# Optimization experiments

Hardware: AMD Instinct MI355X
Metric: run time of the kernel (lower is better)

## Reference

```python
import jax, jax.numpy as jnp
import numpy as np

B, L, D, H = 4, 1024, 256, 8
TEMP = float(np.sqrt(D))
EPS_SM = 1e-6
EPS_LN = 1e-5


def setup_inputs() -> dict:
    key = jax.random.key(0)
    ks = jax.random.split(key, 8)
    std = float(np.sqrt(2.0 / (D * 2)))
    return {
        "q": jax.random.normal(ks[0], (B, L, D), jnp.float32),
        "mask": jax.random.randint(ks[1], (B, L, L), 0, 2, jnp.int32),
        "k": jax.random.normal(ks[2], (B, L, D), jnp.float32),
        "v": jax.random.normal(ks[3], (B, L, D), jnp.float32),
        "w_qs": jax.random.normal(ks[4], (H * D, D), jnp.float32) * std,
        "w_ks": jax.random.normal(ks[5], (H * D, D), jnp.float32) * std,
        "w_vs": jax.random.normal(ks[6], (H * D, D), jnp.float32) * std,
        "fc_w": jax.random.normal(ks[7], (D, H * D), jnp.float32) * float(np.sqrt(2.0 / (D + H * D))),
        "fc_b": jnp.zeros((D,), jnp.float32),
        "ln_g": jnp.ones((D,), jnp.float32),
        "ln_b": jnp.zeros((D,), jnp.float32),
    }


def masked_softmax(x, m):
    # repo's layers.masked_softmax: clamp, mask-mul, stable exp, mask-mul, normalize
    x = jnp.clip(x, -15.0, 15.0) * m
    e = jnp.exp(x - jnp.max(x, axis=-1, keepdims=True)) * m
    return e / (jnp.sum(e, axis=-1, keepdims=True) + EPS_SM)


def reference(q, mask, k, v, w_qs, w_ks, w_vs, fc_w, fc_b, ln_g, ln_b):
    residual = q
    m = mask.astype(q.dtype)[:, None, :, :]          # [B,1,Lq,Lk]
    # projections to per-head full-dim: [B,L,H,D]
    qh = (q @ w_qs.T).reshape(B, L, H, D)
    kh = (k @ w_ks.T).reshape(B, L, H, D)
    vh = (v @ w_vs.T).reshape(B, L, H, D)
    scores = jnp.einsum("bqhd,bkhd->bhqk", qh, kh) / TEMP   # [B,H,Lq,Lk]
    attn = masked_softmax(scores, m)
    out = jnp.einsum("bhqk,bkhd->bqhd", attn, vh).reshape(B, L, H * D)
    out = out @ fc_w.T + fc_b                         # [B,L,D]
    out = out + residual
    mu = jnp.mean(out, axis=-1, keepdims=True)
    var = jnp.var(out, axis=-1, keepdims=True)
    out = (out - mu) / jnp.sqrt(var + EPS_LN) * ln_g + ln_b
    # match torch attn layout: [H*B, Lq, Lk] (head-major)
    attn_hb = jnp.transpose(attn, (1, 0, 2, 3)).reshape(H * B, L, L)
    return out, attn_hb
```

## Files before the change

kernel.cpp:

```cpp
#include <hip/hip_runtime.h>
#include <cstdint>
#include <math.h>

#define Bsz 4
#define Lsz 1024
#define Dsz 256
#define Hsz 8
#define HD  2048
#define NROWS (Bsz*Lsz)
#define INV_TEMP 0.0625f

typedef __attribute__((ext_vector_type(8))) short bf16x8;
typedef __attribute__((ext_vector_type(4))) float f32x4;

__device__ inline unsigned short f2bf(float f) {
    union { float f; unsigned u; } x; x.f = f;
    unsigned r = x.u + 0x7fffu + ((x.u >> 16) & 1u);
    return (unsigned short)(r >> 16);
}
__device__ inline float bf2f(unsigned short u) {
    union { unsigned u; float f; } x; x.u = (unsigned)u << 16; return x.f;
}

#define GBL(p) ((const __attribute__((address_space(1))) unsigned int*)(p))
#define LDS(p) ((__attribute__((address_space(3))) unsigned int*)(p))

template <int TMv, int TNv, typename OutT, int EPI, int MINW>
__global__ __launch_bounds__(256, MINW) void gemm_bt(
    const unsigned short* __restrict__ A, const unsigned short* __restrict__ Bm,
    OutT* __restrict__ C,
    int K, int lda, int ldb, int ldc, int inner,
    long long sA1, long long sA2, long long sB1, long long sB2,
    long long sC1, long long sC2, float alpha,
    const int* __restrict__ mask, long long sM2,
    const float* __restrict__ invs, long long sI1, long long sI2)
{
    constexpr int WMv = TMv / 2, WNv = TNv / 2;
    constexpr int IT = TMv / 32, JT = TNv / 32;
    constexpr int APASS = TMv / 32, NPASS = (TMv + TNv) / 32;

    const int z  = blockIdx.z;
    const int i1 = z / inner;
    const int i2 = z % inner;
    A  += (size_t)i1 * sA1 + (size_t)i2 * sA2;
    Bm += (size_t)i1 * sB1 + (size_t)i2 * sB2;
    C  += (size_t)i1 * sC1 + (size_t)i2 * sC2;
    if (EPI == 1) mask += (size_t)i2 * sM2;
    if (EPI == 2) invs += (size_t)i1 * sI1 + (size_t)i2 * sI2;

    __shared__ unsigned short S[(TMv + TNv) * 64];
    unsigned short* As = S;
    unsigned short* Bs = S + TMv * 64;

    const int t    = threadIdx.x;
    const int lane = t & 63;
    const int w    = t >> 6;
    const int wm   = w & 1;
    const int wn   = w >> 1;
    const int m0   = blockIdx.x * TMv;
    const int n0   = blockIdx.y * TNv;

    const int rA = t >> 3;
    const int ch = (((t & 7) ^ (rA & 7))) * 8;
    const unsigned short* gA = A  + (size_t)(m0 + rA) * lda + ch;
    const unsigned short* gB = Bm + (size_t)(n0 + rA) * ldb + ch;

    const int fr = lane & 15;
    const int q  = lane >> 4;

    f32x4 acc[IT][JT];
#pragma unroll
    for (int i = 0; i < IT; ++i)
#pragma unroll
        for (int j = 0; j < JT; ++j) acc[i][j] = (f32x4){0.f, 0.f, 0.f, 0.f};

    for (int k0 = 0; k0 < K; k0 += 64) {
#pragma unroll
        for (int p = 0; p < NPASS; ++p) {
            const unsigned short* src = (p < APASS)
                ? (gA + (size_t)p * 32 * lda + k0)
                : (gB + (size_t)(p - APASS) * 32 * ldb + k0);
            __builtin_amdgcn_global_load_lds(GBL(src), LDS(S + p * 2048 + t * 8), 16, 0, 0);
        }
        __syncthreads();

#pragma unroll
        for (int ks = 0; ks < 2; ++ks) {
            const int slot = ((ks * 4 + q) ^ (fr & 7)) * 8;
            bf16x8 a[IT], b[JT];
#pragma unroll
            for (int i = 0; i < IT; ++i)
                a[i] = *(const bf16x8*)(As + (wm * WMv + i * 16 + fr) * 64 + slot);
#pragma unroll
            for (int j = 0; j < JT; ++j)
                b[j] = *(const bf16x8*)(Bs + (wn * WNv + j * 16 + fr) * 64 + slot);
#pragma unroll
            for (int i = 0; i < IT; ++i)
#pragma unroll
                for (int j = 0; j < JT; ++j)
                    acc[i][j] = __builtin_amdgcn_mfma_f32_16x16x32_bf16(a[i], b[j], acc[i][j], 0, 0, 0);
        }
        __syncthreads();
    }

#pragma unroll
    for (int i = 0; i < IT; ++i) {
#pragma unroll
        for (int r = 0; r < 4; ++r) {
            const int row = m0 + wm * WMv + i * 16 + q * 4 + r;
#pragma unroll
            for (int j = 0; j < JT; ++j) {
                const int col = n0 + wn * WNv + j * 16 + fr;
                float vv = acc[i][j][r] * alpha;
                if (EPI == 0) {
                    if constexpr (sizeof(OutT) == 4)
                        C[(size_t)row * ldc + col] = (OutT)vv;
                    else
                        ((unsigned short*)C)[(size_t)row * ldc + col] = f2bf(vv);
                } else if (EPI == 1) {
                    const float m = (float)mask[(size_t)row * Lsz + col];
                    vv = fminf(fmaxf(vv, -15.f), 15.f) * m;
                    vv = __expf(vv) * m;
                    ((unsigned short*)C)[(size_t)row * ldc + col] = f2bf(vv);
                } else {
                    vv *= invs[row];
                    ((unsigned short*)C)[(size_t)row * ldc + col] = f2bf(vv);
                }
            }
        }
    }
}

__global__ __launch_bounds__(256) void cast_all(
    const float* __restrict__ q, const float* __restrict__ k, const float* __restrict__ v,
    const float* __restrict__ wq, const float* __restrict__ wk, const float* __restrict__ wv,
    const float* __restrict__ fw,
    unsigned short* __restrict__ qb, unsigned short* __restrict__ kb, unsigned short* __restrict__ vb,
    unsigned short* __restrict__ wqb, unsigned short* __restrict__ wkb, unsigned short* __restrict__ wvb,
    unsigned short* __restrict__ fwb)
{
    const int gid = blockIdx.x * 256 + threadIdx.x;
    const int NQ = 262144;
    const int NW = 131072;
    const float* src; unsigned short* dst; int off;
    if      (gid < NQ)            { src = q;  dst = qb;  off = gid; }
    else if (gid < 2 * NQ)        { src = k;  dst = kb;  off = gid - NQ; }
    else if (gid < 3 * NQ)        { src = v;  dst = vb;  off = gid - 2 * NQ; }
    else if (gid < 3 * NQ + NW)   { src = wq; dst = wqb; off = gid - 3 * NQ; }
    else if (gid < 3 * NQ + 2*NW) { src = wk; dst = wkb; off = gid - 3 * NQ - NW; }
    else if (gid < 3 * NQ + 3*NW) { src = wv; dst = wvb; off = gid - 3 * NQ - 2 * NW; }
    else                          { src = fw; dst = fwb; off = gid - 3 * NQ - 3 * NW; }
    float4 f = ((const float4*)src)[off];
    ushort4 o;
    o.x = f2bf(f.x); o.y = f2bf(f.y); o.z = f2bf(f.z); o.w = f2bf(f.w);
    ((ushort4*)dst)[off] = o;
}

__global__ __launch_bounds__(256) void norm_kernel(const unsigned short* __restrict__ e,
                                                   float* __restrict__ attn,
                                                   float* __restrict__ invsum)
{
    const int r    = blockIdx.x * 4 + (threadIdx.x >> 6);
    const int lane = threadIdx.x & 63;
    const unsigned short* rowp = e + (size_t)r * Lsz + lane * 16;

    union { uint4 v[2]; unsigned short u[16]; } buf;
    buf.v[0] = *(const uint4*)rowp;
    buf.v[1] = *(const uint4*)(rowp + 8);

    float f[16];
    float s = 0.f;
#pragma unroll
    for (int i = 0; i < 16; ++i) { f[i] = bf2f(buf.u[i]); s += f[i]; }
#pragma unroll
    for (int o = 1; o <= 32; o <<= 1) s += __shfl_xor(s, o, 64);
    const float inv = 1.0f / (s + 1e-6f);

    float* op = attn + (size_t)r * Lsz + lane * 16;
#pragma unroll
    for (int c = 0; c < 4; ++c) {
        float4 o4;
        o4.x = f[c * 4 + 0] * inv; o4.y = f[c * 4 + 1] * inv;
        o4.z = f[c * 4 + 2] * inv; o4.w = f[c * 4 + 3] * inv;
        *(float4*)(op + c * 4) = o4;
    }
    if (lane == 0) invsum[r] = inv;
}

__global__ __launch_bounds__(256) void ln_kernel(const float* __restrict__ gout,
                                                 const float* __restrict__ qin,
                                                 const float* __restrict__ fc_b,
                                                 const float* __restrict__ ln_g,
                                                 const float* __restrict__ ln_b,
                                                 float* __restrict__ out)
{
    const int row = blockIdx.x;
    const int t = threadIdx.x;
    const size_t idx = (size_t)row * Dsz + t;
    const size_t P = (size_t)NROWS * Dsz;
    const float val = gout[idx] + gout[idx + P] + gout[idx + 2 * P] + gout[idx + 3 * P]
                    + fc_b[t] + qin[idx];

    __shared__ float red[4];
    float s = val;
#pragma unroll
    for (int o = 32; o > 0; o >>= 1) s += __shfl_down(s, o, 64);
    const int lane = t & 63, w = t >> 6;
    if (lane == 0) red[w] = s;
    __syncthreads();
    const float mu = (red[0] + red[1] + red[2] + red[3]) * (1.0f / Dsz);
    __syncthreads();

    float d = val - mu;
    float s2 = d * d;
#pragma unroll
    for (int o = 32; o > 0; o >>= 1) s2 += __shfl_down(s2, o, 64);
    if (lane == 0) red[w] = s2;
    __syncthreads();
    const float var = (red[0] + red[1] + red[2] + red[3]) * (1.0f / Dsz);

    out[idx] = d * rsqrtf(var + 1e-5f) * ln_g[t] + ln_b[t];
}

extern "C" void kernel_launch(void* const* d_in, const int* in_sizes, int n_in,
                              void* d_out, int out_size, void* d_ws, size_t ws_size,
                              hipStream_t stream)
{
    const float* q    = (const float*)d_in[0];
    const int*   mask = (const int*)d_in[1];
    const float* k    = (const float*)d_in[2];
    const float* v    = (const float*)d_in[3];
    const float* w_qs = (const float*)d_in[4];
    const float* w_ks = (const float*)d_in[5];
    const float* w_vs = (const float*)d_in[6];
    const float* fc_w = (const float*)d_in[7];
    const float* fc_b = (const float*)d_in[8];
    const float* ln_g = (const float*)d_in[9];
    const float* ln_b = (const float*)d_in[10];

    float* out  = (float*)d_out;
    float* attn = (float*)d_out + (size_t)NROWS * Dsz;

    unsigned short* wsu = (unsigned short*)d_ws;
    unsigned short* qh     = wsu;
    unsigned short* kh     = qh + (size_t)NROWS * HD;
    unsigned short* q_bf   = kh + (size_t)NROWS * HD;
    unsigned short* k_bf   = q_bf + (size_t)NROWS * Dsz;
    unsigned short* v_bf   = k_bf + (size_t)NROWS * Dsz;
    unsigned short* wq_bf  = v_bf + (size_t)NROWS * Dsz;
    unsigned short* wk_bf  = wq_bf + (size_t)HD * Dsz;
    unsigned short* wv_bf  = wk_bf + (size_t)HD * Dsz;
    unsigned short* vt     = wv_bf + (size_t)HD * Dsz;
    unsigned short* attn_e = vt + (size_t)Bsz * HD * Lsz;
    unsigned short* attnv  = attn_e + (size_t)32 * Lsz * Lsz;
    unsigned short* fcw_bf = attnv + (size_t)NROWS * HD;
    float*          invsum = (float*)(fcw_bf + (size_t)Dsz * HD);
    float*          fcout  = invsum + 32768;

    dim3 blk(256);

    cast_all<<<dim3(5120), blk, 0, stream>>>(q, k, v, w_qs, w_ks, w_vs, fc_w,
                                             q_bf, k_bf, v_bf, wq_bf, wk_bf, wv_bf, fcw_bf);

    {
        dim3 grid(NROWS / 64, HD / 256, 2);
        gemm_bt<64, 256, unsigned short, 0, 3><<<grid, blk, 0, stream>>>(q_bf, wq_bf, qh,
            Dsz, Dsz, Dsz, HD, 2,
            0, (long long)NROWS * Dsz, 0, (long long)HD * Dsz, 0, (long long)NROWS * HD,
            1.0f, nullptr, 0, nullptr, 0, 0);
    }

    {
        dim3 grid(HD / 64, Lsz / 256, Bsz);
        gemm_bt<64, 256, unsigned short, 0, 3><<<grid, blk, 0, stream>>>(wv_bf, v_bf, vt,
            Dsz, Dsz, Dsz, Lsz, 1,
            0, 0, (long long)Lsz * Dsz, 0, (long long)HD * Lsz, 0,
            1.0f, nullptr, 0, nullptr, 0, 0);
    }

    {
        dim3 grid(Lsz / 128, Lsz / 256, Hsz * Bsz);
        gemm_bt<128, 256, unsigned short, 1, 2><<<grid, blk, 0, stream>>>(qh, kh, attn_e,
            Dsz, HD, HD, Lsz, Bsz,
            Dsz, (long long)Lsz * HD, Dsz, (long long)Lsz * HD,
            (long long)Bsz * Lsz * Lsz, (long long)Lsz * Lsz,
            INV_TEMP, mask, (long long)Lsz * Lsz, nullptr, 0, 0);
    }

    norm_kernel<<<dim3(32 * Lsz / 4), blk, 0, stream>>>(attn_e, attn, invsum);

    {
        dim3 grid(Lsz / 64, Dsz / 256, Hsz * Bsz);
        gemm_bt<64, 256, unsigned short, 2, 3><<<grid, blk, 0, stream>>>(attn_e, vt, attnv,
            Lsz, Lsz, Lsz, HD, Bsz,
            (long long)Bsz * Lsz * Lsz, (long long)Lsz * Lsz,
            (long long)Dsz * Lsz, (long long)HD * Lsz,
            Dsz, (long long)Lsz * HD,
            1.0f, nullptr, 0, invsum, (long long)Bsz * Lsz, (long long)Lsz);
    }

    {
        dim3 grid(NROWS / 64, Dsz / 256, 4);
        gemm_bt<64, 256, float, 0, 3><<<grid, blk, 0, stream>>>(attnv, fcw_bf, fcout,
            512, HD, HD, Dsz, 4,
            0, 512, 0, 512, 0, (long long)NROWS * Dsz,
            1.0f, nullptr, 0, nullptr, 0, 0);
    }

    ln_kernel<<<dim3(NROWS), blk, 0, stream>>>(fcout, q, fc_b, ln_g, ln_b, out);
}
```

Measured before the change: 349.4 us.

## Add double-buffered LDS pipelining, bf16 mask precast, and retune GEMM tiles

Adds an optional double-buffered main loop to the shared GEMM kernel, so the global-to-LDS load of the next K tile is issued while the current tile is multiplied, removing one barrier per iteration. The int32 mask is converted to a bf16 0/1 array inside the cast kernel, which halves the mask bytes the score GEMM epilogue reads. Tile shapes for all GEMMs change to 128x128 (64x128 for the fc projection) with adjusted occupancy hints. The double-buffered variant doubles LDS per block, which may lower occupancy, and the cast kernel now also reads the full 4M-element mask.

```diff
diff --git a/kernel.cpp b/kernel.cpp
--- a/kernel.cpp
+++ b/kernel.cpp
@@ -25,19 +25,20 @@
 #define GBL(p) ((const __attribute__((address_space(1))) unsigned int*)(p))
 #define LDS(p) ((__attribute__((address_space(3))) unsigned int*)(p))
 
-template <int TMv, int TNv, typename OutT, int EPI, int MINW>
+template <int TMv, int TNv, typename OutT, int EPI, int MINW, int DB>
 __global__ __launch_bounds__(256, MINW) void gemm_bt(
     const unsigned short* __restrict__ A, const unsigned short* __restrict__ Bm,
     OutT* __restrict__ C,
     int K, int lda, int ldb, int ldc, int inner,
     long long sA1, long long sA2, long long sB1, long long sB2,
     long long sC1, long long sC2, float alpha,
-    const int* __restrict__ mask, long long sM2,
+    const unsigned short* __restrict__ maskb, long long sM2,
     const float* __restrict__ invs, long long sI1, long long sI2)
 {
     constexpr int WMv = TMv / 2, WNv = TNv / 2;
     constexpr int IT = TMv / 32, JT = TNv / 32;
     constexpr int APASS = TMv / 32, NPASS = (TMv + TNv) / 32;
+    constexpr int TILE = (TMv + TNv) * 64;
 
     const int z  = blockIdx.z;
     const int i1 = z / inner;
@@ -45,12 +46,10 @@
     A  += (size_t)i1 * sA1 + (size_t)i2 * sA2;
     Bm += (size_t)i1 * sB1 + (size_t)i2 * sB2;
     C  += (size_t)i1 * sC1 + (size_t)i2 * sC2;
-    if (EPI == 1) mask += (size_t)i2 * sM2;
-    if (EPI == 2) invs += (size_t)i1 * sI1 + (size_t)i2 * sI2;
-
-    __shared__ unsigned short S[(TMv + TNv) * 64];
-    unsigned short* As = S;
-    unsigned short* Bs = S + TMv * 64;
+    if (EPI == 1) maskb += (size_t)i2 * sM2;
+    if (EPI == 2) invs  += (size_t)i1 * sI1 + (size_t)i2 * sI2;
+
+    __shared__ unsigned short S[(DB ? 2 : 1) * TILE];
 
     const int t    = threadIdx.x;
     const int lane = t & 63;
@@ -61,7 +60,7 @@
     const int n0   = blockIdx.y * TNv;
 
     const int rA = t >> 3;
-    const int ch = (((t & 7) ^ (rA & 7))) * 8;
+    const int ch = ((t & 7) ^ (rA & 7)) * 8;
     const unsigned short* gA = A  + (size_t)(m0 + rA) * lda + ch;
     const unsigned short* gB = Bm + (size_t)(n0 + rA) * ldb + ch;
 
@@ -74,16 +73,17 @@
 #pragma unroll
         for (int j = 0; j < JT; ++j) acc[i][j] = (f32x4){0.f, 0.f, 0.f, 0.f};
 
-    for (int k0 = 0; k0 < K; k0 += 64) {
+    auto stage = [&](unsigned short* Sb, int k0) {
 #pragma unroll
         for (int p = 0; p < NPASS; ++p) {
             const unsigned short* src = (p < APASS)
                 ? (gA + (size_t)p * 32 * lda + k0)
                 : (gB + (size_t)(p - APASS) * 32 * ldb + k0);
-            __builtin_amdgcn_global_load_lds(GBL(src), LDS(S + p * 2048 + t * 8), 16, 0, 0);
-        }
-        __syncthreads();
-
+            __builtin_amdgcn_global_load_lds(GBL(src), LDS(Sb + p * 2048 + t * 8), 16, 0, 0);
+        }
+    };
+    auto kstep = [&](const unsigned short* As) {
+        const unsigned short* Bs = As + TMv * 64;
 #pragma unroll
         for (int ks = 0; ks < 2; ++ks) {
             const int slot = ((ks * 4 + q) ^ (fr & 7)) * 8;
@@ -100,7 +100,26 @@
                 for (int j = 0; j < JT; ++j)
                     acc[i][j] = __builtin_amdgcn_mfma_f32_16x16x32_bf16(a[i], b[j], acc[i][j], 0, 0, 0);
         }
+    };
+
+    if constexpr (DB) {
+        const int nk = K >> 6;
+        stage(S, 0);
         __syncthreads();
+        int cur = 0;
+        for (int kt = 0; kt < nk; ++kt) {
+            if (kt + 1 < nk) stage(S + (cur ^ 1) * TILE, (kt + 1) << 6);
+            kstep(S + cur * TILE);
+            __syncthreads();
+            cur ^= 1;
+        }
+    } else {
+        for (int k0 = 0; k0 < K; k0 += 64) {
+            stage(S, k0);
+            __syncthreads();
+            kstep(S);
+            __syncthreads();
+        }
     }
 
 #pragma unroll
@@ -118,7 +137,7 @@
                     else
                         ((unsigned short*)C)[(size_t)row * ldc + col] = f2bf(vv);
                 } else if (EPI == 1) {
-                    const float m = (float)mask[(size_t)row * Lsz + col];
+                    const float m = bf2f(maskb[(size_t)row * Lsz + col]);
                     vv = fminf(fmaxf(vv, -15.f), 15.f) * m;
                     vv = __expf(vv) * m;
                     ((unsigned short*)C)[(size_t)row * ldc + col] = f2bf(vv);
@@ -134,14 +153,26 @@
 __global__ __launch_bounds__(256) void cast_all(
     const float* __restrict__ q, const float* __restrict__ k, const float* __restrict__ v,
     const float* __restrict__ wq, const float* __restrict__ wk, const float* __restrict__ wv,
-    const float* __restrict__ fw,
+    const float* __restrict__ fw, const int* __restrict__ mask,
     unsigned short* __restrict__ qb, unsigned short* __restrict__ kb, unsigned short* __restrict__ vb,
     unsigned short* __restrict__ wqb, unsigned short* __restrict__ wkb, unsigned short* __restrict__ wvb,
-    unsigned short* __restrict__ fwb)
+    unsigned short* __restrict__ fwb, unsigned short* __restrict__ mb)
 {
     const int gid = blockIdx.x * 256 + threadIdx.x;
     const int NQ = 262144;
     const int NW = 131072;
+    const int NF = 3 * NQ + 4 * NW;
+    if (gid >= NF) {
+        const int off = gid - NF;
+        const int4 mi = ((const int4*)mask)[off];
+        ushort4 o;
+        o.x = mi.x ? 0x3F80 : 0;
+        o.y = mi.y ? 0x3F80 : 0;
+        o.z = mi.z ? 0x3F80 : 0;
+        o.w = mi.w ? 0x3F80 : 0;
+        ((ushort4*)mb)[off] = o;
+        return;
+    }
     const float* src; unsigned short* dst; int off;
     if      (gid < NQ)            { src = q;  dst = qb;  off = gid; }
     else if (gid < 2 * NQ)        { src = k;  dst = kb;  off = gid - NQ; }
@@ -256,42 +287,43 @@
     unsigned short* fcw_bf = attnv + (size_t)NROWS * HD;
     float*          invsum = (float*)(fcw_bf + (size_t)Dsz * HD);
     float*          fcout  = invsum + 32768;
+    unsigned short* maskb  = (unsigned short*)(fcout + (size_t)4 * NROWS * Dsz);
 
     dim3 blk(256);
 
-    cast_all<<<dim3(5120), blk, 0, stream>>>(q, k, v, w_qs, w_ks, w_vs, fc_w,
-                                             q_bf, k_bf, v_bf, wq_bf, wk_bf, wv_bf, fcw_bf);
-
-    {
-        dim3 grid(NROWS / 64, HD / 256, 2);
-        gemm_bt<64, 256, unsigned short, 0, 3><<<grid, blk, 0, stream>>>(q_bf, wq_bf, qh,
+    cast_all<<<dim3(9216), blk, 0, stream>>>(q, k, v, w_qs, w_ks, w_vs, fc_w, mask,
+                                             q_bf, k_bf, v_bf, wq_bf, wk_bf, wv_bf, fcw_bf, maskb);
+
+    {
+        dim3 grid(NROWS / 128, HD / 128, 2);
+        gemm_bt<128, 128, unsigned short, 0, 3, 0><<<grid, blk, 0, stream>>>(q_bf, wq_bf, qh,
             Dsz, Dsz, Dsz, HD, 2,
             0, (long long)NROWS * Dsz, 0, (long long)HD * Dsz, 0, (long long)NROWS * HD,
             1.0f, nullptr, 0, nullptr, 0, 0);
     }
 
     {
-        dim3 grid(HD / 64, Lsz / 256, Bsz);
-        gemm_bt<64, 256, unsigned short, 0, 3><<<grid, blk, 0, stream>>>(wv_bf, v_bf, vt,
+        dim3 grid(HD / 128, Lsz / 128, Bsz);
+        gemm_bt<128, 128, unsigned short, 0, 2, 1><<<grid, blk, 0, stream>>>(wv_bf, v_bf, vt,
             Dsz, Dsz, Dsz, Lsz, 1,
             0, 0, (long long)Lsz * Dsz, 0, (long long)HD * Lsz, 0,
             1.0f, nullptr, 0, nullptr, 0, 0);
     }
 
     {
-        dim3 grid(Lsz / 128, Lsz / 256, Hsz * Bsz);
-        gemm_bt<128, 256, unsigned short, 1, 2><<<grid, blk, 0, stream>>>(qh, kh, attn_e,
+        dim3 grid(Lsz / 128, Lsz / 128, Hsz * Bsz);
+        gemm_bt<128, 128, unsigned short, 1, 3, 0><<<grid, blk, 0, stream>>>(qh, kh, attn_e,
             Dsz, HD, HD, Lsz, Bsz,
             Dsz, (long long)Lsz * HD, Dsz, (long long)Lsz * HD,
             (long long)Bsz * Lsz * Lsz, (long long)Lsz * Lsz,
-            INV_TEMP, mask, (long long)Lsz * Lsz, nullptr, 0, 0);
+            INV_TEMP, maskb, (long long)Lsz * Lsz, nullptr, 0, 0);
     }
 
     norm_kernel<<<dim3(32 * Lsz / 4), blk, 0, stream>>>(attn_e, attn, invsum);
 
     {
-        dim3 grid(Lsz / 64, Dsz / 256, Hsz * Bsz);
-        gemm_bt<64, 256, unsigned short, 2, 3><<<grid, blk, 0, stream>>>(attn_e, vt, attnv,
+        dim3 grid(Lsz / 128, Dsz / 128, Hsz * Bsz);
+        gemm_bt<128, 128, unsigned short, 2, 2, 1><<<grid, blk, 0, stream>>>(attn_e, vt, attnv,
             Lsz, Lsz, Lsz, HD, Bsz,
             (long long)Bsz * Lsz * Lsz, (long long)Lsz * Lsz,
             (long long)Dsz * Lsz, (long long)HD * Lsz,
@@ -300,8 +332,8 @@
     }
 
     {
-        dim3 grid(NROWS / 64, Dsz / 256, 4);
-        gemm_bt<64, 256, float, 0, 3><<<grid, blk, 0, stream>>>(attnv, fcw_bf, fcout,
+        dim3 grid(NROWS / 64, Dsz / 128, 4);
+        gemm_bt<64, 128, float, 0, 3, 1><<<grid, blk, 0, stream>>>(attnv, fcw_bf, fcout,
             512, HD, HD, Dsz, 4,
             0, 512, 0, 512, 0, (long long)NROWS * Dsz,
             1.0f, nullptr, 0, nullptr, 0, 0);
```

After: 336.8 us. 1.04x faster.
